# Kernel optimization log

Measured on AMD Instinct MI355X. Metric: run time of the kernel, lower is better.

The kernel has to match this reference:

```python
import jax, jax.numpy as jnp
import numpy as np

N = 50000   # nodes
E = 800000  # edges (before self-loops)
DIN = 128
H, C = 4, 32
HC = H * C  # 128
DE = 3      # edge feature dim
G = 64      # graphs in batch
HID = 32
DOUT = 1
LN_EPS = 1e-5


def setup_inputs() -> dict:
    key = jax.random.key(0)
    ks = iter(jax.random.split(key, 64))
    def nrm(shape, s=0.1):
        return jax.random.normal(next(ks), shape, dtype=jnp.float32) * s
    inp = {}
    inp["x"] = jax.random.normal(next(ks), (N, DIN), dtype=jnp.float32)
    inp["edge_index"] = jax.random.randint(next(ks), (2, E), 0, N, dtype=jnp.int32)
    inp["batch"] = jnp.sort(jax.random.randint(next(ks), (N,), 0, G, dtype=jnp.int32))
    inp["edge_attr"] = jax.random.normal(next(ks), (E, DE), dtype=jnp.float32)
    # GATv2 layers: layer0 in=DIN(128); layers 1,2 in=HC(128)
    for l, din in enumerate([DIN, HC, HC]):
        inp[f"Wl{l}"] = nrm((HC, din)); inp[f"bl{l}"] = jnp.zeros((HC,), jnp.float32)
        inp[f"Wr{l}"] = nrm((HC, din)); inp[f"br{l}"] = jnp.zeros((HC,), jnp.float32)
        inp[f"We{l}"] = nrm((HC, DE))
        inp[f"att{l}"] = nrm((H, C))
        inp[f"bo{l}"] = jnp.zeros((HC,), jnp.float32)
    for l in range(2):
        inp[f"ln{l}_g"] = jnp.ones((HC,), jnp.float32)
        inp[f"ln{l}_b"] = jnp.zeros((HC,), jnp.float32)
    # post-processing MLP: 128->32->32->32->1
    inp["pw1"] = nrm((HID, HC)); inp["pb1"] = jnp.zeros((HID,), jnp.float32)
    inp["pw2"] = nrm((HID, HID)); inp["pb2"] = jnp.zeros((HID,), jnp.float32)
    inp["pw3"] = nrm((HID, HID)); inp["pb3"] = jnp.zeros((HID,), jnp.float32)
    inp["pw4"] = nrm((DOUT, HID)); inp["pb4"] = jnp.zeros((DOUT,), jnp.float32)
    return inp


def _gat_layer(x, src, dst, eattr, Wl, bl, Wr, br, We, att, bo):
    # GATv2Conv (concat heads). x_l from lin_l -> source, x_r from lin_r -> target.
    xl = (x @ Wl.T + bl).reshape(-1, H, C)
    xr = (x @ Wr.T + br).reshape(-1, H, C)
    e = (eattr @ We.T).reshape(-1, H, C)
    m = jax.nn.leaky_relu(xl[src] + xr[dst] + e, negative_slope=0.2)  # [E',H,C]
    s = jnp.einsum('ehc,hc->eh', m, att)                              # [E',H]
    smax = jax.ops.segment_max(s, dst, num_segments=N)
    ex = jnp.exp(s - smax[dst])
    den = jax.ops.segment_sum(ex, dst, num_segments=N)
    alpha = ex / (den[dst] + 1e-16)
    out = jax.ops.segment_sum(alpha[:, :, None] * xl[src], dst, num_segments=N)
    return out.reshape(-1, HC) + bo


def _ln(x, g, b):
    mu = jnp.mean(x, axis=-1, keepdims=True)
    var = jnp.mean((x - mu) ** 2, axis=-1, keepdims=True)
    return (x - mu) * jax.lax.rsqrt(var + LN_EPS) * g + b


def _forward(x, edge_attr, edge_index, batch, p):
    src0, dst0 = edge_index[0], edge_index[1]
    # PyG add_self_loops with fill_value='mean': per-dst-node mean of edge_attr
    cnt = jax.ops.segment_sum(jnp.ones((E,), jnp.float32), dst0, num_segments=N)
    loop_attr = jax.ops.segment_sum(edge_attr, dst0, num_segments=N) / jnp.maximum(cnt, 1.0)[:, None]
    ar = jnp.arange(N, dtype=src0.dtype)
    src = jnp.concatenate([src0, ar]); dst = jnp.concatenate([dst0, ar])
    ea = jnp.concatenate([edge_attr, loop_attr], axis=0)
    embedding = x
    for l in range(3):
        x = _gat_layer(x, src, dst, ea, p[f"Wl{l}"], p[f"bl{l}"], p[f"Wr{l}"],
                       p[f"br{l}"], p[f"We{l}"], p[f"att{l}"], p[f"bo{l}"])
        embedding = x
        x = jax.nn.relu(x)  # dropout inactive (eval)
        if l != 2:
            x = _ln(x, p[f"ln{l}_g"], p[f"ln{l}_b"])
    pooled = jax.ops.segment_max(x, batch, num_segments=G)
    pooled = jnp.where(jnp.isfinite(pooled), pooled, 0.0)
    h = jax.nn.relu(pooled @ p["pw1"].T + p["pb1"])
    h = jax.nn.relu(h @ p["pw2"].T + p["pb2"])
    h = jax.nn.relu(h @ p["pw3"].T + p["pb3"])
    out = h @ p["pw4"].T + p["pb4"]
    return embedding, out


def reference(x, edge_index, batch, edge_attr,
              Wl0, bl0, Wr0, br0, We0, att0, bo0,
              Wl1, bl1, Wr1, br1, We1, att1, bo1,
              Wl2, bl2, Wr2, br2, We2, att2, bo2,
              ln0_g, ln0_b, ln1_g, ln1_b,
              pw1, pb1, pw2, pb2, pw3, pb3, pw4, pb4):
    p = dict(Wl0=Wl0, bl0=bl0, Wr0=Wr0, br0=br0, We0=We0, att0=att0, bo0=bo0,
             Wl1=Wl1, bl1=bl1, Wr1=Wr1, br1=br1, We1=We1, att1=att1, bo1=bo1,
             Wl2=Wl2, bl2=bl2, Wr2=Wr2, br2=br2, We2=We2, att2=att2, bo2=bo2,
             ln0_g=ln0_g, ln0_b=ln0_b, ln1_g=ln1_g, ln1_b=ln1_b,
             pw1=pw1, pb1=pb1, pw2=pw2, pb2=pb2, pw3=pw3, pb3=pb3, pw4=pw4, pb4=pb4)
    return _forward(x, edge_attr, edge_index, batch, p)
```

## Files before the change

### kernel.cpp

```cpp
#include <hip/hip_runtime.h>
#include <math.h>


#define LN_EPS 1e-5f
#define LOG2E 1.44269504088896340736f
#define CHUNK 4096
#define BCAP 8192

typedef short bf16x8 __attribute__((ext_vector_type(8)));
typedef float f32x4 __attribute__((ext_vector_type(4)));
typedef float f32x2 __attribute__((ext_vector_type(2)));

static __device__ __forceinline__ unsigned short f2bf(float f) {
  unsigned int u = __float_as_uint(f);
  u += 0x7fffu + ((u >> 16) & 1u);
  return (unsigned short)(u >> 16);
}

static __device__ __forceinline__ float dpp_sum8(float v) {
  int x;
  x = __builtin_amdgcn_update_dpp(0, __float_as_int(v), 0x0B1, 0xf, 0xf, true);
  v += __int_as_float(x);
  x = __builtin_amdgcn_update_dpp(0, __float_as_int(v), 0x04E, 0xf, 0xf, true);
  v += __int_as_float(x);
  x = __builtin_amdgcn_update_dpp(0, __float_as_int(v), 0x141, 0xf, 0xf, true);
  v += __int_as_float(x);
  return v;
}


__global__ __launch_bounds__(256) void k_binA(const int* __restrict__ ei, const float* __restrict__ ea,
                                              int* __restrict__ gcnt, float4* __restrict__ staged,
                                              int E, int nbuk) {
  __shared__ int hist[256];
  __shared__ int basebuf[256];
  int t = threadIdx.x;
  int e0 = blockIdx.x * CHUNK;

  hist[t] = 0;
  __syncthreads();
#pragma unroll
  for (int i = 0; i < CHUNK / 256; ++i) {
    int e = e0 + i * 256 + t;
    if (e < E) atomicAdd(&hist[ei[E + e] >> 8], 1);
  }
  __syncthreads();
  int h = hist[t];
  if (t < nbuk && h > 0) basebuf[t] = t * BCAP + atomicAdd(&gcnt[t], h);
  hist[t] = 0;
  __syncthreads();
#pragma unroll
  for (int i = 0; i < CHUNK / 256; ++i) {
    int e = e0 + i * 256 + t;
    if (e < E) {
      int s = ei[e];
      int d = ei[E + e];
      int b = d >> 8;
      int r = atomicAdd(&hist[b], 1);
      float4 rec;
      rec.x = ea[e * 3 + 0];
      rec.y = ea[e * 3 + 1];
      rec.z = ea[e * 3 + 2];
      rec.w = __int_as_float(s | (d << 16));
      staged[basebuf[b] + r] = rec;
    }
  }
}

__global__ void k_bscan(const int* __restrict__ gcnt, int* __restrict__ bukStart,
                        int* __restrict__ offs, int N, int nbuk, int EP) {
  __shared__ int sh[256];
  int t = threadIdx.x;
  int nodes = (t < nbuk) ? min(256, N - t * 256) : 0;
  int v = (t < nbuk) ? gcnt[t] + nodes : 0;
  sh[t] = v;
  __syncthreads();
  for (int d = 1; d < 256; d <<= 1) {
    int add = (t >= d) ? sh[t - d] : 0;
    __syncthreads();
    sh[t] += add;
    __syncthreads();
  }
  if (t < nbuk) bukStart[t] = sh[t] - v;
  if (t == 0) offs[N] = EP;
}

__global__ __launch_bounds__(256) void k_binB(const float4* __restrict__ staged,
                                              const int* __restrict__ gcnt,
                                              const int* __restrict__ bukStart,
                                              float4* __restrict__ e4,
                                              int* __restrict__ offs, int N) {
  __shared__ int hist[256], cur[256], begS[256], sh[256];
  int t = threadIdx.x;
  int b = blockIdx.x;
  int n0 = b * 256;
  int nn = min(256, N - n0);
  int m = gcnt[b];
  size_t sbase = (size_t)b * BCAP;

  hist[t] = 0;
  __syncthreads();
  for (int p = t; p < m; p += 256) {
    unsigned int u = (unsigned int)__float_as_int(staged[sbase + p].w);
    atomicAdd(&hist[(int)(u >> 16) - n0], 1);
  }
  __syncthreads();
  int v = (t < nn) ? hist[t] + 1 : 0;
  sh[t] = v;
  __syncthreads();
  for (int d = 1; d < 256; d <<= 1) {
    int add = (t >= d) ? sh[t - d] : 0;
    __syncthreads();
    sh[t] += add;
    __syncthreads();
  }
  if (t < nn) {
    int base = bukStart[b] + sh[t] - v;
    cur[t] = base;
    begS[t] = base;
    offs[n0 + t] = base;
  }
  __syncthreads();
  for (int p = t; p < m; p += 256) {
    float4 rec = staged[sbase + p];
    unsigned int u = (unsigned int)__float_as_int(rec.w);
    int pos = atomicAdd(&cur[(int)(u >> 16) - n0], 1);
    rec.w = __int_as_float((int)(u & 0xffffu) * 256);
    e4[pos] = rec;
  }
  __syncthreads();
  if (t < nn) {
    int beg = begS[t], last = cur[t];
    float s0 = 0.f, s1 = 0.f, s2 = 0.f;
    for (int p = beg; p < last; ++p) {
      float4 r = e4[p];
      s0 += r.x;
      s1 += r.y;
      s2 += r.z;
    }
    float invc = 1.0f / fmaxf((float)(last - beg), 1.0f);
    float4 r;
    r.x = s0 * invc;
    r.y = s1 * invc;
    r.z = s2 * invc;
    r.w = __int_as_float((n0 + t) * 256);
    e4[last] = r;
  }
}


__global__ void k_convx(const float* __restrict__ x, unsigned short* __restrict__ xb, int n) {
  int i = (blockIdx.x * blockDim.x + threadIdx.x) * 4;
  if (i >= n) return;
  float4 v = *(const float4*)&x[i];
  ushort4 o;
  o.x = f2bf(v.x); o.y = f2bf(v.y); o.z = f2bf(v.z); o.w = f2bf(v.w);
  *(ushort4*)&xb[i] = o;
}

__global__ void k_convW(const float* __restrict__ w0, const float* __restrict__ w1,
                        const float* __restrict__ w2, const float* __restrict__ w3,
                        const float* __restrict__ w4, const float* __restrict__ w5,
                        unsigned short* __restrict__ dst) {
  const float* srcs[6] = {w0, w1, w2, w3, w4, w5};
  const float* s = srcs[blockIdx.y];
  int i = blockIdx.x * 256 + threadIdx.x;
  dst[(size_t)blockIdx.y * 16384 + i] = f2bf(s[i]);
}

__global__ void k_pack(const float* __restrict__ We0, const float* __restrict__ att0,
                       const float* __restrict__ We1, const float* __restrict__ att1,
                       const float* __restrict__ We2, const float* __restrict__ att2,
                       float* __restrict__ tab) {
  int l = blockIdx.x;
  int t = threadIdx.x;
  const float* We = (l == 0) ? We0 : ((l == 1) ? We1 : We2);
  const float* att = (l == 0) ? att0 : ((l == 1) ? att1 : att2);
  float* o = tab + (size_t)l * 512 + t * 16;
#pragma unroll
  for (int j = 0; j < 4; ++j) {
    o[j] = We[(t * 4 + j) * 3 + 0];
    o[4 + j] = We[(t * 4 + j) * 3 + 1];
    o[8 + j] = We[(t * 4 + j) * 3 + 2];
    o[12 + j] = att[t * 4 + j] * LOG2E;
  }
}

__global__ __launch_bounds__(256) void k_gemm_mfma(const unsigned short* __restrict__ xb,
                                                   const unsigned short* __restrict__ Wb,
                                                   const float* __restrict__ bl, const float* __restrict__ br,
                                                   unsigned short* __restrict__ xlb,
                                                   unsigned short* __restrict__ xrb, int N) {
  int wave = threadIdx.x >> 6;
  int lane = threadIdx.x & 63;
  int which = blockIdx.y;
  const unsigned short* W = Wb + (size_t)which * 16384;
  const float* bias = which ? br : bl;
  unsigned short* out = which ? xrb : xlb;

  int row0 = (blockIdx.x * 4 + wave) * 16;
  if (row0 >= N) return;
  int m = lane & 15;
  int q = lane >> 4;

  int brow = row0 + m;
  if (brow >= N) brow = N - 1;
  const unsigned short* xrow = xb + (size_t)brow * 128 + q * 8;

  bf16x8 bfrag[4];
#pragma unroll
  for (int kt = 0; kt < 4; ++kt) bfrag[kt] = *(const bf16x8*)(xrow + kt * 32);

  f32x4 acc[8];
#pragma unroll
  for (int jt = 0; jt < 8; ++jt) acc[jt] = (f32x4){0.f, 0.f, 0.f, 0.f};

  const unsigned short* wbase = W + (size_t)m * 128 + q * 8;
#pragma unroll
  for (int kt = 0; kt < 4; ++kt) {
#pragma unroll
    for (int jt = 0; jt < 8; ++jt) {
      bf16x8 a = *(const bf16x8*)(wbase + (size_t)jt * 16 * 128 + kt * 32);
      acc[jt] = __builtin_amdgcn_mfma_f32_16x16x32_bf16(a, bfrag[kt], acc[jt], 0, 0, 0);
    }
  }

  int node = row0 + m;
  if (node < N) {
    unsigned short* orow = out + (size_t)node * 128 + q * 4;
#pragma unroll
    for (int jt = 0; jt < 8; ++jt) {
      float4 bs = *(const float4*)&bias[jt * 16 + q * 4];
      uint2 pack;
      pack.x = (unsigned int)f2bf(acc[jt][0] + bs.x) | ((unsigned int)f2bf(acc[jt][1] + bs.y) << 16);
      pack.y = (unsigned int)f2bf(acc[jt][2] + bs.z) | ((unsigned int)f2bf(acc[jt][3] + bs.w) << 16);
      *(uint2*)(orow + jt * 16) = pack;
    }
  }
}

__global__ __launch_bounds__(256) void k_agg(const unsigned short* __restrict__ xlb,
                                             const unsigned short* __restrict__ xrb,
                                             const float4* __restrict__ e4,
                                             const int* __restrict__ offs,
                                             const float* __restrict__ scoreTab,
                                             const float* __restrict__ bo,
                                             const float* __restrict__ lng, const float* __restrict__ lnb,
                                             unsigned short* __restrict__ xnext_bf,
                                             float* __restrict__ emb, int last, int N) {
  int w = (blockIdx.x * blockDim.x + threadIdx.x) >> 6;
  if (w >= N) return;
  int lane = threadIdx.x & 63;
  int half = lane >> 5;
  int sl = lane & 31;
  int c = sl * 4;
  unsigned int c2 = (unsigned int)(c * 2);
  int beg = offs[w], end = offs[w + 1];
  int cnt = end - beg;

  f32x2 xr01, xr23, wea01, wea23, web01, web23, wec01, wec23, at01, at23;
  {
    const float4* tp = (const float4*)(scoreTab + (size_t)sl * 16);
    float4 pa = tp[0], pb = tp[1], pc = tp[2], pt = tp[3];
    wea01[0] = pa.x; wea01[1] = pa.y; wea23[0] = pa.z; wea23[1] = pa.w;
    web01[0] = pb.x; web01[1] = pb.y; web23[0] = pb.z; web23[1] = pb.w;
    wec01[0] = pc.x; wec01[1] = pc.y; wec23[0] = pc.z; wec23[1] = pc.w;
    at01[0] = pt.x; at01[1] = pt.y; at23[0] = pt.z; at23[1] = pt.w;
    uint2 vr = *(const uint2*)&xrb[(size_t)w * 128 + c];
    xr01[0] = __uint_as_float(vr.x << 16);
    xr01[1] = __uint_as_float(vr.x & 0xffff0000u);
    xr23[0] = __uint_as_float(vr.y << 16);
    xr23[1] = __uint_as_float(vr.y & 0xffff0000u);
  }

  const char* xlB = (const char*)xlb;
  const char* e4B = (const char*)e4;
  unsigned int lastoff = (unsigned int)(end - 1) << 4;

  float l = 0.f;
  f32x2 acc01 = {0.f, 0.f}, acc23 = {0.f, 0.f};

  int T = (cnt + 1) >> 1;

  unsigned int o0 = (unsigned int)(beg + half) << 4;
  if (o0 > lastoff) o0 = lastoff;
  unsigned int o1 = o0 + 32u;
  if (o1 > lastoff) o1 = lastoff;
  unsigned int o2 = o1 + 32u;
  if (o2 > lastoff) o2 = lastoff;
  float4 e0 = *(const float4*)(e4B + o0);
  float4 e1 = *(const float4*)(e4B + o1);
  float4 e2 = *(const float4*)(e4B + o2);
  uint2 g0 = *(const uint2*)(xlB + ((unsigned int)__float_as_int(e0.w) + c2));
  uint2 g1 = *(const uint2*)(xlB + ((unsigned int)__float_as_int(e1.w) + c2));
  unsigned int offP = o2;

  auto compute = [&](const float4& e, uint2 v, bool valid) {
    f32x2 xl01, xl23;
    xl01[0] = __uint_as_float(v.x << 16);
    xl01[1] = __uint_as_float(v.x & 0xffff0000u);
    xl23[0] = __uint_as_float(v.y << 16);
    xl23[1] = __uint_as_float(v.y & 0xffff0000u);
    f32x2 ex = {e.x, e.x}, ey = {e.y, e.y}, ez = {e.z, e.z};
    f32x2 t01 = __builtin_elementwise_fma(wea01, ex,
                  __builtin_elementwise_fma(web01, ey,
                    __builtin_elementwise_fma(wec01, ez, xr01 + xl01)));
    f32x2 t23 = __builtin_elementwise_fma(wea23, ex,
                  __builtin_elementwise_fma(web23, ey,
                    __builtin_elementwise_fma(wec23, ez, xr23 + xl23)));
    t01 = __builtin_elementwise_max(t01, t01 * 0.2f);
    t23 = __builtin_elementwise_max(t23, t23 * 0.2f);
    f32x2 d2 = __builtin_elementwise_fma(t01, at01, t23 * at23);
    float s = d2[0] + d2[1];
    float wgt = __builtin_amdgcn_exp2f(dpp_sum8(s));
    if (!valid) wgt = 0.f;
    l += wgt;
    f32x2 w2 = {wgt, wgt};
    acc01 = __builtin_elementwise_fma(xl01, w2, acc01);
    acc23 = __builtin_elementwise_fma(xl23, w2, acc23);
  };

#pragma unroll 2
  for (int it = 0; it < T - 3; ++it) {
    unsigned int o3 = offP + 32u;
    if (o3 > lastoff) o3 = lastoff;
    float4 e3 = *(const float4*)(e4B + o3);
    uint2 g2 = *(const uint2*)(xlB + ((unsigned int)__float_as_int(e2.w) + c2));
    compute(e0, g0, true);
    e0 = e1; e1 = e2; e2 = e3;
    g0 = g1; g1 = g2;
    offP = o3;
  }
  if (T >= 3) {
    uint2 g2 = *(const uint2*)(xlB + ((unsigned int)__float_as_int(e2.w) + c2));
    compute(e0, g0, true);
    e0 = e1; e1 = e2;
    g0 = g1; g1 = g2;
  }
  if (T >= 2) {
    compute(e0, g0, true);
    e0 = e1;
    g0 = g1;
  }
  {
    int idx = 2 * (T - 1) + half;
    compute(e0, g0, idx < cnt);
  }

  l += __shfl_xor(l, 32);
  float a0 = acc01[0]; a0 += __shfl_xor(a0, 32);
  float a1 = acc01[1]; a1 += __shfl_xor(a1, 32);
  float a2 = acc23[0]; a2 += __shfl_xor(a2, 32);
  float a3 = acc23[1]; a3 += __shfl_xor(a3, 32);

  float inv = 1.0f / l;
  f32x4 o;
  const float4 bo4 = *(const float4*)&bo[c];
  o[0] = a0 * inv + bo4.x;
  o[1] = a1 * inv + bo4.y;
  o[2] = a2 * inv + bo4.z;
  o[3] = a3 * inv + bo4.w;

  if (last) {
    if (half == 0) {
      float4 st = {o[0], o[1], o[2], o[3]};
      *(float4*)&emb[(size_t)w * 128 + c] = st;
    }
  } else {
    f32x4 r;
    r[0] = fmaxf(o[0], 0.f);
    r[1] = fmaxf(o[1], 0.f);
    r[2] = fmaxf(o[2], 0.f);
    r[3] = fmaxf(o[3], 0.f);
    float s = r[0] + r[1] + r[2] + r[3];
    s += __shfl_xor(s, 1);
    s += __shfl_xor(s, 2);
    s += __shfl_xor(s, 4);
    s += __shfl_xor(s, 8);
    s += __shfl_xor(s, 16);
    float mu = s * 0.0078125f;
    f32x4 d;
    d[0] = r[0] - mu;
    d[1] = r[1] - mu;
    d[2] = r[2] - mu;
    d[3] = r[3] - mu;
    float v2 = d[0] * d[0] + d[1] * d[1] + d[2] * d[2] + d[3] * d[3];
    v2 += __shfl_xor(v2, 1);
    v2 += __shfl_xor(v2, 2);
    v2 += __shfl_xor(v2, 4);
    v2 += __shfl_xor(v2, 8);
    v2 += __shfl_xor(v2, 16);
    float var = v2 * 0.0078125f;
    float rstd = rsqrtf(var + LN_EPS);
    if (half == 0) {
      const float4 g4 = *(const float4*)&lng[c];
      const float4 b4 = *(const float4*)&lnb[c];
      float o0 = d[0] * rstd * g4.x + b4.x;
      float o1 = d[1] * rstd * g4.y + b4.y;
      float o2 = d[2] * rstd * g4.z + b4.z;
      float o3 = d[3] * rstd * g4.w + b4.w;
      uint2 pack;
      pack.x = (unsigned int)f2bf(o0) | ((unsigned int)f2bf(o1) << 16);
      pack.y = (unsigned int)f2bf(o2) | ((unsigned int)f2bf(o3) << 16);
      *(uint2*)&xnext_bf[(size_t)w * 128 + c] = pack;
    }
  }
}

__global__ void k_pool(const float* __restrict__ emb, const int* __restrict__ batch,
                       float* __restrict__ pooled, int N) {
  int c = threadIdx.x & 127;
  int half = threadIdx.x >> 7;
  int base = blockIdx.x * 64 + half;
  int limit = min(blockIdx.x * 64 + 64, N);
  float cur = 0.f;
  int curg = -1;
  for (int n = base; n < limit; n += 2) {
    int g = batch[n];
    if (g != curg) {
      if (curg >= 0) atomicMax((unsigned int*)&pooled[curg * 128 + c], __float_as_uint(cur));
      curg = g;
      cur = 0.f;
    }
    cur = fmaxf(cur, emb[(size_t)n * 128 + c]);
  }
  if (curg >= 0) atomicMax((unsigned int*)&pooled[curg * 128 + c], __float_as_uint(cur));
}

__global__ void k_mlp(const float* __restrict__ pooled,
                      const float* __restrict__ pw1, const float* __restrict__ pb1,
                      const float* __restrict__ pw2, const float* __restrict__ pb2,
                      const float* __restrict__ pw3, const float* __restrict__ pb3,
                      const float* __restrict__ pw4, const float* __restrict__ pb4,
                      float* __restrict__ out) {
  int g = blockIdx.x;
  int t = threadIdx.x;
  __shared__ float buf1[32], buf2[32];
  if (t < 32) {
    float acc = pb1[t];
    for (int k = 0; k < 128; ++k) acc += pw1[t * 128 + k] * pooled[g * 128 + k];
    buf1[t] = fmaxf(acc, 0.f);
  }
  __syncthreads();
  if (t < 32) {
    float acc = pb2[t];
    for (int k = 0; k < 32; ++k) acc += pw2[t * 32 + k] * buf1[k];
    buf2[t] = fmaxf(acc, 0.f);
  }
  __syncthreads();
  if (t < 32) {
    float acc = pb3[t];
    for (int k = 0; k < 32; ++k) acc += pw3[t * 32 + k] * buf2[k];
    buf1[t] = fmaxf(acc, 0.f);
  }
  __syncthreads();
  if (t == 0) {
    float acc = pb4[0];
    for (int k = 0; k < 32; ++k) acc += pw4[k] * buf1[k];
    out[g] = acc;
  }
}


extern "C" void kernel_launch(void* const* d_in, const int* in_sizes, int n_in,
                              void* d_out, int out_size, void* d_ws, size_t ws_size,
                              hipStream_t stream) {
  const float* x_in = (const float*)d_in[0];
  const int* ei = (const int*)d_in[1];
  const int* batch = (const int*)d_in[2];
  const float* ea = (const float*)d_in[3];

  const int N = in_sizes[0] / 128;
  const int E = in_sizes[1] / 2;
  const int EP = E + N;
  const int G = out_size - N * 128;
  const int NBUK = (N + 255) / 256;

  const float *Wl[3], *bl[3], *Wr[3], *br[3], *We[3], *att[3], *bo[3];
  for (int l = 0; l < 3; ++l) {
    Wl[l] = (const float*)d_in[4 + 7 * l];
    bl[l] = (const float*)d_in[5 + 7 * l];
    Wr[l] = (const float*)d_in[6 + 7 * l];
    br[l] = (const float*)d_in[7 + 7 * l];
    We[l] = (const float*)d_in[8 + 7 * l];
    att[l] = (const float*)d_in[9 + 7 * l];
    bo[l] = (const float*)d_in[10 + 7 * l];
  }
  const float* lng[2] = {(const float*)d_in[25], (const float*)d_in[27]};
  const float* lnb[2] = {(const float*)d_in[26], (const float*)d_in[28]};
  const float* pw1 = (const float*)d_in[29];
  const float* pb1 = (const float*)d_in[30];
  const float* pw2 = (const float*)d_in[31];
  const float* pb2 = (const float*)d_in[32];
  const float* pw3 = (const float*)d_in[33];
  const float* pb3 = (const float*)d_in[34];
  const float* pw4 = (const float*)d_in[35];
  const float* pb4 = (const float*)d_in[36];

  char* base = (char*)d_ws;
  size_t cur = 0;
  auto carve = [&](size_t bytes) -> char* {
    char* p = base + cur;
    cur += (bytes + 255) & ~(size_t)255;
    return p;
  };
  unsigned short* xlb = (unsigned short*)carve((size_t)N * 128 * 2);
  unsigned short* xrb = (unsigned short*)carve((size_t)N * 128 * 2);
  unsigned short* xb = (unsigned short*)carve((size_t)N * 128 * 2);
  unsigned short* Wb = (unsigned short*)carve((size_t)6 * 16384 * 2);
  float4* e4 = (float4*)carve((size_t)EP * 16);
  float4* staged = (float4*)carve((size_t)NBUK * BCAP * 16);
  int* offs = (int*)carve((size_t)(N + 1) * 4);
  int* gcnt = (int*)carve((size_t)NBUK * 4);
  int* bukStart = (int*)carve((size_t)(NBUK + 1) * 4);
  float* scoreTab = (float*)carve((size_t)3 * 512 * 4);
  float* pooled = (float*)carve((size_t)G * 128 * 4);

  float* emb_out = (float*)d_out;
  float* mlp_out = (float*)d_out + (size_t)N * 128;

  hipMemsetAsync(gcnt, 0, (size_t)NBUK * 4, stream);
  hipMemsetAsync(pooled, 0, (size_t)G * 128 * 4, stream);

  k_binA<<<(E + CHUNK - 1) / CHUNK, 256, 0, stream>>>(ei, ea, gcnt, staged, E, NBUK);
  k_bscan<<<1, 256, 0, stream>>>(gcnt, bukStart, offs, N, NBUK, EP);
  k_binB<<<NBUK, 256, 0, stream>>>(staged, gcnt, bukStart, e4, offs, N);

  k_convx<<<(N * 128 / 4 + 255) / 256, 256, 0, stream>>>(x_in, xb, N * 128);
  {
    dim3 g(64, 6);
    k_convW<<<g, 256, 0, stream>>>(Wl[0], Wr[0], Wl[1], Wr[1], Wl[2], Wr[2], Wb);
  }
  k_pack<<<3, 32, 0, stream>>>(We[0], att[0], We[1], att[1], We[2], att[2], scoreTab);

  for (int l = 0; l < 3; ++l) {
    dim3 ggrid((N + 63) / 64, 2);
    k_gemm_mfma<<<ggrid, 256, 0, stream>>>(xb, Wb + (size_t)l * 32768, bl[l], br[l], xlb, xrb, N);
    int last = (l == 2) ? 1 : 0;
    const float* g = last ? bo[l] : lng[l];
    const float* b = last ? bo[l] : lnb[l];
    k_agg<<<(N * 64 + 255) / 256, 256, 0, stream>>>(xlb, xrb, e4, offs,
                                                    scoreTab + (size_t)l * 512,
                                                    bo[l], g, b,
                                                    xb, emb_out, last, N);
  }

  k_pool<<<(N + 63) / 64, 256, 0, stream>>>(emb_out, batch, pooled, N);
  k_mlp<<<G, 64, 0, stream>>>(pooled, pw1, pb1, pw2, pb2, pw3, pb3, pw4, pb4, mlp_out);
}
```

Baseline: 496.6 us.

## Fuse preprocessing kernels and compute both GATv2 projections in one GEMM

Merges edge binning, weight conversion to bf16 and score-table packing into one multi-role launch, which removes two kernel launches. The layer-0 GEMM now reads the fp32 input and converts it to bf16 itself, so the separate conversion pass over x is gone. Each GEMM wave computes the left and right projections together, so the input fragment is loaded once and reused for both. It also pads e4 with eight zero records written in k_bscan, and doubles the accumulator registers per wave, which may lower occupancy.

```diff
diff --git a/kernel.cpp b/kernel.cpp
--- a/kernel.cpp
+++ b/kernel.cpp
@@ -29,46 +29,79 @@
 }
 
 
-__global__ __launch_bounds__(256) void k_binA(const int* __restrict__ ei, const float* __restrict__ ea,
-                                              int* __restrict__ gcnt, float4* __restrict__ staged,
-                                              int E, int nbuk) {
+__global__ __launch_bounds__(256) void k_pre(
+    const int* __restrict__ ei, const float* __restrict__ ea,
+    int* __restrict__ gcnt, float4* __restrict__ staged, int E, int nbuk, int nbinA,
+    const float* __restrict__ w0, const float* __restrict__ w1,
+    const float* __restrict__ w2, const float* __restrict__ w3,
+    const float* __restrict__ w4, const float* __restrict__ w5,
+    unsigned short* __restrict__ Wb,
+    const float* __restrict__ We0, const float* __restrict__ att0,
+    const float* __restrict__ We1, const float* __restrict__ att1,
+    const float* __restrict__ We2, const float* __restrict__ att2,
+    float* __restrict__ tab) {
   __shared__ int hist[256];
   __shared__ int basebuf[256];
+  int b = blockIdx.x;
   int t = threadIdx.x;
-  int e0 = blockIdx.x * CHUNK;
-
-  hist[t] = 0;
-  __syncthreads();
-#pragma unroll
-  for (int i = 0; i < CHUNK / 256; ++i) {
-    int e = e0 + i * 256 + t;
-    if (e < E) atomicAdd(&hist[ei[E + e] >> 8], 1);
-  }
-  __syncthreads();
-  int h = hist[t];
-  if (t < nbuk && h > 0) basebuf[t] = t * BCAP + atomicAdd(&gcnt[t], h);
-  hist[t] = 0;
-  __syncthreads();
-#pragma unroll
-  for (int i = 0; i < CHUNK / 256; ++i) {
-    int e = e0 + i * 256 + t;
-    if (e < E) {
-      int s = ei[e];
-      int d = ei[E + e];
-      int b = d >> 8;
-      int r = atomicAdd(&hist[b], 1);
-      float4 rec;
-      rec.x = ea[e * 3 + 0];
-      rec.y = ea[e * 3 + 1];
-      rec.z = ea[e * 3 + 2];
-      rec.w = __int_as_float(s | (d << 16));
-      staged[basebuf[b] + r] = rec;
+
+  if (b < nbinA) {
+    int e0 = b * CHUNK;
+    hist[t] = 0;
+    __syncthreads();
+#pragma unroll
+    for (int i = 0; i < CHUNK / 256; ++i) {
+      int e = e0 + i * 256 + t;
+      if (e < E) atomicAdd(&hist[ei[E + e] >> 8], 1);
+    }
+    __syncthreads();
+    int h = hist[t];
+    if (t < nbuk && h > 0) basebuf[t] = t * BCAP + atomicAdd(&gcnt[t], h);
+    hist[t] = 0;
+    __syncthreads();
+#pragma unroll
+    for (int i = 0; i < CHUNK / 256; ++i) {
+      int e = e0 + i * 256 + t;
+      if (e < E) {
+        int s = ei[e];
+        int d = ei[E + e];
+        int bk = d >> 8;
+        int r = atomicAdd(&hist[bk], 1);
+        float4 rec;
+        rec.x = ea[e * 3 + 0];
+        rec.y = ea[e * 3 + 1];
+        rec.z = ea[e * 3 + 2];
+        rec.w = __int_as_float(s | (d << 16));
+        staged[basebuf[bk] + r] = rec;
+      }
+    }
+  } else if (b < nbinA + 384) {
+    int bb = b - nbinA;
+    const float* srcs[6] = {w0, w1, w2, w3, w4, w5};
+    int mtx = bb >> 6;
+    int i = (bb & 63) * 256 + t;
+    Wb[(size_t)mtx * 16384 + i] = f2bf(srcs[mtx][i]);
+  } else {
+    if (t < 96) {
+      int l = t >> 5;
+      int sl = t & 31;
+      const float* We = (l == 0) ? We0 : ((l == 1) ? We1 : We2);
+      const float* att = (l == 0) ? att0 : ((l == 1) ? att1 : att2);
+      float* o = tab + (size_t)l * 512 + sl * 16;
+#pragma unroll
+      for (int j = 0; j < 4; ++j) {
+        o[j] = We[(sl * 4 + j) * 3 + 0];
+        o[4 + j] = We[(sl * 4 + j) * 3 + 1];
+        o[8 + j] = We[(sl * 4 + j) * 3 + 2];
+        o[12 + j] = att[sl * 4 + j] * LOG2E;
+      }
     }
   }
 }
 
 __global__ void k_bscan(const int* __restrict__ gcnt, int* __restrict__ bukStart,
-                        int* __restrict__ offs, int N, int nbuk, int EP) {
+                        int* __restrict__ offs, float4* __restrict__ e4,
+                        int N, int nbuk, int EP) {
   __shared__ int sh[256];
   int t = threadIdx.x;
   int nodes = (t < nbuk) ? min(256, N - t * 256) : 0;
@@ -83,6 +116,12 @@
   }
   if (t < nbuk) bukStart[t] = sh[t] - v;
   if (t == 0) offs[N] = EP;
+  if (t < 8) {
+    float4 r;
+    r.x = 0.f; r.y = 0.f; r.z = 0.f;
+    r.w = __int_as_float(0);
+    e4[EP + t] = r;
+  }
 }
 
 __global__ __launch_bounds__(256) void k_binB(const float4* __restrict__ staged,
@@ -148,55 +187,18 @@
   }
 }
 
-
-__global__ void k_convx(const float* __restrict__ x, unsigned short* __restrict__ xb, int n) {
-  int i = (blockIdx.x * blockDim.x + threadIdx.x) * 4;
-  if (i >= n) return;
-  float4 v = *(const float4*)&x[i];
-  ushort4 o;
-  o.x = f2bf(v.x); o.y = f2bf(v.y); o.z = f2bf(v.z); o.w = f2bf(v.w);
-  *(ushort4*)&xb[i] = o;
-}
-
-__global__ void k_convW(const float* __restrict__ w0, const float* __restrict__ w1,
-                        const float* __restrict__ w2, const float* __restrict__ w3,
-                        const float* __restrict__ w4, const float* __restrict__ w5,
-                        unsigned short* __restrict__ dst) {
-  const float* srcs[6] = {w0, w1, w2, w3, w4, w5};
-  const float* s = srcs[blockIdx.y];
-  int i = blockIdx.x * 256 + threadIdx.x;
-  dst[(size_t)blockIdx.y * 16384 + i] = f2bf(s[i]);
-}
-
-__global__ void k_pack(const float* __restrict__ We0, const float* __restrict__ att0,
-                       const float* __restrict__ We1, const float* __restrict__ att1,
-                       const float* __restrict__ We2, const float* __restrict__ att2,
-                       float* __restrict__ tab) {
-  int l = blockIdx.x;
-  int t = threadIdx.x;
-  const float* We = (l == 0) ? We0 : ((l == 1) ? We1 : We2);
-  const float* att = (l == 0) ? att0 : ((l == 1) ? att1 : att2);
-  float* o = tab + (size_t)l * 512 + t * 16;
-#pragma unroll
-  for (int j = 0; j < 4; ++j) {
-    o[j] = We[(t * 4 + j) * 3 + 0];
-    o[4 + j] = We[(t * 4 + j) * 3 + 1];
-    o[8 + j] = We[(t * 4 + j) * 3 + 2];
-    o[12 + j] = att[t * 4 + j] * LOG2E;
-  }
-}
-
-__global__ __launch_bounds__(256) void k_gemm_mfma(const unsigned short* __restrict__ xb,
-                                                   const unsigned short* __restrict__ Wb,
-                                                   const float* __restrict__ bl, const float* __restrict__ br,
-                                                   unsigned short* __restrict__ xlb,
-                                                   unsigned short* __restrict__ xrb, int N) {
+template <bool F32IN>
+__global__ __launch_bounds__(256) void k_gemm_fused(const float* __restrict__ xf,
+                                                    const unsigned short* __restrict__ xb,
+                                                    const unsigned short* __restrict__ Wb,
+                                                    const float* __restrict__ bl,
+                                                    const float* __restrict__ br,
+                                                    unsigned short* __restrict__ xlb,
+                                                    unsigned short* __restrict__ xrb, int N) {
   int wave = threadIdx.x >> 6;
   int lane = threadIdx.x & 63;
-  int which = blockIdx.y;
-  const unsigned short* W = Wb + (size_t)which * 16384;
-  const float* bias = which ? br : bl;
-  unsigned short* out = which ? xrb : xlb;
+  const unsigned short* WL = Wb;
+  const unsigned short* WR = Wb + 16384;
 
   int row0 = (blockIdx.x * 4 + wave) * 16;
   if (row0 >= N) return;
@@ -205,36 +207,63 @@
 
   int brow = row0 + m;
   if (brow >= N) brow = N - 1;
-  const unsigned short* xrow = xb + (size_t)brow * 128 + q * 8;
 
   bf16x8 bfrag[4];
-#pragma unroll
-  for (int kt = 0; kt < 4; ++kt) bfrag[kt] = *(const bf16x8*)(xrow + kt * 32);
-
-  f32x4 acc[8];
-#pragma unroll
-  for (int jt = 0; jt < 8; ++jt) acc[jt] = (f32x4){0.f, 0.f, 0.f, 0.f};
-
-  const unsigned short* wbase = W + (size_t)m * 128 + q * 8;
+  if constexpr (F32IN) {
+    const float* xrow = xf + (size_t)brow * 128 + q * 8;
+#pragma unroll
+    for (int kt = 0; kt < 4; ++kt) {
+      float4 u0 = *(const float4*)(xrow + kt * 32);
+      float4 u1 = *(const float4*)(xrow + kt * 32 + 4);
+      bf16x8 f;
+      f[0] = (short)f2bf(u0.x); f[1] = (short)f2bf(u0.y);
+      f[2] = (short)f2bf(u0.z); f[3] = (short)f2bf(u0.w);
+      f[4] = (short)f2bf(u1.x); f[5] = (short)f2bf(u1.y);
+      f[6] = (short)f2bf(u1.z); f[7] = (short)f2bf(u1.w);
+      bfrag[kt] = f;
+    }
+  } else {
+    const unsigned short* xrow = xb + (size_t)brow * 128 + q * 8;
+#pragma unroll
+    for (int kt = 0; kt < 4; ++kt) bfrag[kt] = *(const bf16x8*)(xrow + kt * 32);
+  }
+
+  f32x4 accL[8], accR[8];
+#pragma unroll
+  for (int jt = 0; jt < 8; ++jt) {
+    accL[jt] = (f32x4){0.f, 0.f, 0.f, 0.f};
+    accR[jt] = (f32x4){0.f, 0.f, 0.f, 0.f};
+  }
+
+  const unsigned short* wl = WL + (size_t)m * 128 + q * 8;
+  const unsigned short* wr = WR + (size_t)m * 128 + q * 8;
 #pragma unroll
   for (int kt = 0; kt < 4; ++kt) {
 #pragma unroll
     for (int jt = 0; jt < 8; ++jt) {
-      bf16x8 a = *(const bf16x8*)(wbase + (size_t)jt * 16 * 128 + kt * 32);
-      acc[jt] = __builtin_amdgcn_mfma_f32_16x16x32_bf16(a, bfrag[kt], acc[jt], 0, 0, 0);
+      bf16x8 aL = *(const bf16x8*)(wl + (size_t)jt * 2048 + kt * 32);
+      accL[jt] = __builtin_amdgcn_mfma_f32_16x16x32_bf16(aL, bfrag[kt], accL[jt], 0, 0, 0);
+      bf16x8 aR = *(const bf16x8*)(wr + (size_t)jt * 2048 + kt * 32);
+      accR[jt] = __builtin_amdgcn_mfma_f32_16x16x32_bf16(aR, bfrag[kt], accR[jt], 0, 0, 0);
     }
   }
 
   int node = row0 + m;
   if (node < N) {
-    unsigned short* orow = out + (size_t)node * 128 + q * 4;
+    unsigned short* ol = xlb + (size_t)node * 128 + q * 4;
+    unsigned short* orr = xrb + (size_t)node * 128 + q * 4;
 #pragma unroll
     for (int jt = 0; jt < 8; ++jt) {
-      float4 bs = *(const float4*)&bias[jt * 16 + q * 4];
-      uint2 pack;
-      pack.x = (unsigned int)f2bf(acc[jt][0] + bs.x) | ((unsigned int)f2bf(acc[jt][1] + bs.y) << 16);
-      pack.y = (unsigned int)f2bf(acc[jt][2] + bs.z) | ((unsigned int)f2bf(acc[jt][3] + bs.w) << 16);
-      *(uint2*)(orow + jt * 16) = pack;
+      float4 bsL = *(const float4*)&bl[jt * 16 + q * 4];
+      uint2 pL;
+      pL.x = (unsigned int)f2bf(accL[jt][0] + bsL.x) | ((unsigned int)f2bf(accL[jt][1] + bsL.y) << 16);
+      pL.y = (unsigned int)f2bf(accL[jt][2] + bsL.z) | ((unsigned int)f2bf(accL[jt][3] + bsL.w) << 16);
+      *(uint2*)(ol + jt * 16) = pL;
+      float4 bsR = *(const float4*)&br[jt * 16 + q * 4];
+      uint2 pR;
+      pR.x = (unsigned int)f2bf(accR[jt][0] + bsR.x) | ((unsigned int)f2bf(accR[jt][1] + bsR.y) << 16);
+      pR.y = (unsigned int)f2bf(accR[jt][2] + bsR.z) | ((unsigned int)f2bf(accR[jt][3] + bsR.w) << 16);
+      *(uint2*)(orr + jt * 16) = pR;
     }
   }
 }
@@ -273,13 +302,13 @@
     xr23[1] = __uint_as_float(vr.y & 0xffff0000u);
   }
 
+  const char* e4B = (const char*)e4;
   const char* xlB = (const char*)xlb;
-  const char* e4B = (const char*)e4;
-  unsigned int lastoff = (unsigned int)(end - 1) << 4;
 
   float l = 0.f;
   f32x2 acc01 = {0.f, 0.f}, acc23 = {0.f, 0.f};
 
+  unsigned int lastoff = (unsigned int)(end - 1) << 4;
   int T = (cnt + 1) >> 1;
 
   unsigned int o0 = (unsigned int)(beg + half) << 4;
@@ -354,24 +383,24 @@
   float a3 = acc23[1]; a3 += __shfl_xor(a3, 32);
 
   float inv = 1.0f / l;
-  f32x4 o;
+  f32x4 o4;
   const float4 bo4 = *(const float4*)&bo[c];
-  o[0] = a0 * inv + bo4.x;
-  o[1] = a1 * inv + bo4.y;
-  o[2] = a2 * inv + bo4.z;
-  o[3] = a3 * inv + bo4.w;
+  o4[0] = a0 * inv + bo4.x;
+  o4[1] = a1 * inv + bo4.y;
+  o4[2] = a2 * inv + bo4.z;
+  o4[3] = a3 * inv + bo4.w;
 
   if (last) {
     if (half == 0) {
-      float4 st = {o[0], o[1], o[2], o[3]};
+      float4 st = {o4[0], o4[1], o4[2], o4[3]};
       *(float4*)&emb[(size_t)w * 128 + c] = st;
     }
   } else {
     f32x4 r;
-    r[0] = fmaxf(o[0], 0.f);
-    r[1] = fmaxf(o[1], 0.f);
-    r[2] = fmaxf(o[2], 0.f);
-    r[3] = fmaxf(o[3], 0.f);
+    r[0] = fmaxf(o4[0], 0.f);
+    r[1] = fmaxf(o4[1], 0.f);
+    r[2] = fmaxf(o4[2], 0.f);
+    r[3] = fmaxf(o4[3], 0.f);
     float s = r[0] + r[1] + r[2] + r[3];
     s += __shfl_xor(s, 1);
     s += __shfl_xor(s, 2);
@@ -475,6 +504,7 @@
   const int EP = E + N;
   const int G = out_size - N * 128;
   const int NBUK = (N + 255) / 256;
+  const int NBINA = (E + CHUNK - 1) / CHUNK;
 
   const float *Wl[3], *bl[3], *Wr[3], *br[3], *We[3], *att[3], *bo[3];
   for (int l = 0; l < 3; ++l) {
@@ -508,7 +538,7 @@
   unsigned short* xrb = (unsigned short*)carve((size_t)N * 128 * 2);
   unsigned short* xb = (unsigned short*)carve((size_t)N * 128 * 2);
   unsigned short* Wb = (unsigned short*)carve((size_t)6 * 16384 * 2);
-  float4* e4 = (float4*)carve((size_t)EP * 16);
+  float4* e4 = (float4*)carve((size_t)(EP + 8) * 16);
   float4* staged = (float4*)carve((size_t)NBUK * BCAP * 16);
   int* offs = (int*)carve((size_t)(N + 1) * 4);
   int* gcnt = (int*)carve((size_t)NBUK * 4);
@@ -522,20 +552,21 @@
   hipMemsetAsync(gcnt, 0, (size_t)NBUK * 4, stream);
   hipMemsetAsync(pooled, 0, (size_t)G * 128 * 4, stream);
 
-  k_binA<<<(E + CHUNK - 1) / CHUNK, 256, 0, stream>>>(ei, ea, gcnt, staged, E, NBUK);
-  k_bscan<<<1, 256, 0, stream>>>(gcnt, bukStart, offs, N, NBUK, EP);
+  k_pre<<<NBINA + 384 + 1, 256, 0, stream>>>(ei, ea, gcnt, staged, E, NBUK, NBINA,
+                                             Wl[0], Wr[0], Wl[1], Wr[1], Wl[2], Wr[2], Wb,
+                                             We[0], att[0], We[1], att[1], We[2], att[2],
+                                             scoreTab);
+  k_bscan<<<1, 256, 0, stream>>>(gcnt, bukStart, offs, e4, N, NBUK, EP);
   k_binB<<<NBUK, 256, 0, stream>>>(staged, gcnt, bukStart, e4, offs, N);
 
-  k_convx<<<(N * 128 / 4 + 255) / 256, 256, 0, stream>>>(x_in, xb, N * 128);
-  {
-    dim3 g(64, 6);
-    k_convW<<<g, 256, 0, stream>>>(Wl[0], Wr[0], Wl[1], Wr[1], Wl[2], Wr[2], Wb);
-  }
-  k_pack<<<3, 32, 0, stream>>>(We[0], att[0], We[1], att[1], We[2], att[2], scoreTab);
-
   for (int l = 0; l < 3; ++l) {
-    dim3 ggrid((N + 63) / 64, 2);
-    k_gemm_mfma<<<ggrid, 256, 0, stream>>>(xb, Wb + (size_t)l * 32768, bl[l], br[l], xlb, xrb, N);
+    dim3 ggrid((N + 63) / 64);
+    if (l == 0) {
+      k_gemm_fused<true><<<ggrid, 256, 0, stream>>>(x_in, xb, Wb, bl[0], br[0], xlb, xrb, N);
+    } else {
+      k_gemm_fused<false><<<ggrid, 256, 0, stream>>>(nullptr, xb, Wb + (size_t)l * 32768,
+                                                     bl[l], br[l], xlb, xrb, N);
+    }
     int last = (l == 2) ? 1 : 0;
     const float* g = last ? bo[l] : lng[l];
     const float* b = last ? bo[l] : lnb[l];
```

New measurement: 505.8 us. About the same (+1.8%).
